# Kernel optimization log

Hardware: AMD Instinct MI355X
Metric: run time of the kernel (lower is better)

Reference implementation:

```python
import jax, jax.numpy as jnp
import numpy as np

N_NODES = 100000
N_EDGES = 1600000
IN_FEATS = 128
HIDDEN = 32
HEADS = 4
OUT_FEATS = 64
NEG_SLOPE = 0.2  # DGL GATConv default negative_slope


def gat_layer(x, src, dst, fc_w, attn_l, attn_r, bias, n_nodes):
    """DGL GATConv: fc -> per-node attn terms -> edge leaky_relu -> segment softmax -> scatter-sum.
    x: [N, F_in]; fc_w: [F_in, H*D]; attn_l/attn_r: [H, D]; bias: [H*D].
    Returns [N, H, D]."""
    H, D = attn_l.shape
    feat = (x @ fc_w).reshape(-1, H, D)            # [N, H, D]
    el = jnp.sum(feat * attn_l, axis=-1)           # [N, H]
    er = jnp.sum(feat * attn_r, axis=-1)           # [N, H]
    e = jax.nn.leaky_relu(el[src] + er[dst], NEG_SLOPE)   # [E, H]
    # segment softmax over incoming edges of each dst node
    m = jax.ops.segment_max(e, dst, num_segments=n_nodes)  # [N, H] (-inf for 0-in-degree)
    ex = jnp.exp(e - m[dst])                       # [E, H]
    denom = jax.ops.segment_sum(ex, dst, num_segments=n_nodes)  # [N, H]
    alpha = ex / denom[dst]                        # [E, H]
    msg = feat[src] * alpha[:, :, None]            # [E, H, D]
    out = jax.ops.segment_sum(msg, dst, num_segments=n_nodes)   # [N, H, D]
    return out + bias.reshape(1, H, D)


def setup_inputs() -> dict:
    key = jax.random.key(0)
    ks = jax.random.split(key, 12)
    features = jax.random.normal(ks[0], (N_NODES, IN_FEATS), dtype=jnp.float32)
    src = jax.random.randint(ks[1], (N_EDGES,), 0, N_NODES)
    dst = jax.random.randint(ks[2], (N_EDGES,), 0, N_NODES)
    s1 = 1.0 / np.sqrt(IN_FEATS)
    s2 = 1.0 / np.sqrt(HIDDEN * HEADS)
    fc1_w = jax.random.normal(ks[3], (IN_FEATS, HIDDEN * HEADS), dtype=jnp.float32) * s1
    attn_l1 = jax.random.normal(ks[4], (HEADS, HIDDEN), dtype=jnp.float32) * s1
    attn_r1 = jax.random.normal(ks[5], (HEADS, HIDDEN), dtype=jnp.float32) * s1
    bias1 = jnp.zeros((HIDDEN * HEADS,), dtype=jnp.float32)
    fc2_w = jax.random.normal(ks[6], (HIDDEN * HEADS, OUT_FEATS), dtype=jnp.float32) * s2
    attn_l2 = jax.random.normal(ks[7], (1, OUT_FEATS), dtype=jnp.float32) * s2
    attn_r2 = jax.random.normal(ks[8], (1, OUT_FEATS), dtype=jnp.float32) * s2
    bias2 = jnp.zeros((OUT_FEATS,), dtype=jnp.float32)
    return {"features": features, "src": src, "dst": dst,
            "fc1_w": fc1_w, "attn_l1": attn_l1, "attn_r1": attn_r1, "bias1": bias1,
            "fc2_w": fc2_w, "attn_l2": attn_l2, "attn_r2": attn_r2, "bias2": bias2}


def reference(features, src, dst, fc1_w, attn_l1, attn_r1, bias1, fc2_w, attn_l2, attn_r2, bias2):
    n = features.shape[0]
    x = gat_layer(features, src, dst, fc1_w, attn_l1, attn_r1, bias1, n)  # [N, H, D1]
    x = jax.nn.elu(x.reshape(n, -1))                                     # [N, H*D1]
    x = gat_layer(x, src, dst, fc2_w, attn_l2, attn_r2, bias2, n)        # [N, 1, D2]
    return x.mean(axis=1)                                                # [N, D2]
```

## Files before the change

kernel.cpp:

```cpp
#include <hip/hip_runtime.h>
#include <math.h>

typedef __attribute__((ext_vector_type(8))) short bf16x8;
typedef __attribute__((ext_vector_type(4))) float f32x4;

#define MAXDEG 64


__device__ __forceinline__ unsigned int packbf2(float a, float b) {
    unsigned int ua = __float_as_uint(a);
    ua = (ua + 0x7FFFu + ((ua >> 16) & 1u)) >> 16;
    unsigned int ub = __float_as_uint(b);
    ub = (ub + 0x7FFFu + ((ub >> 16) & 1u)) & 0xFFFF0000u;
    return ua | ub;
}

__device__ __forceinline__ unsigned short bf16r(float x) {
    unsigned int u = __float_as_uint(x);
    u = (u + 0x7FFFu + ((u >> 16) & 1u)) >> 16;
    return (unsigned short)u;
}

__device__ __forceinline__ void bf2_fma(unsigned int u, float w, float& a0, float& a1) {
    a0 += w * __uint_as_float(u << 16);
    a1 += w * __uint_as_float(u & 0xFFFF0000u);
}


__global__ __launch_bounds__(256) void k_gemm1_rank(const int* __restrict__ dst,
                                                    int* __restrict__ cnt,
                                                    int* __restrict__ rank, int e,
                                                    const float* __restrict__ X,
                                                    const float* __restrict__ W,
                                                    const float* __restrict__ attn_l,
                                                    const float* __restrict__ attn_r,
                                                    unsigned short* __restrict__ feat,
                                                    float* __restrict__ el,
                                                    float* __restrict__ er, int n) {
    __shared__ unsigned short sX[64 * 128];
    __shared__ unsigned short sWT[128 * 128];
    int t = threadIdx.x;
    int ebase = blockIdx.x * 1024 + t;
    int d0 = (ebase < e) ? dst[ebase] : -1;
    int d1 = (ebase + 256 < e) ? dst[ebase + 256] : -1;
    int d2 = (ebase + 512 < e) ? dst[ebase + 512] : -1;
    int d3 = (ebase + 768 < e) ? dst[ebase + 768] : -1;

    int node0 = blockIdx.x * 64;
    {
        const float4* Xv = (const float4*)X;
        char* sXb = (char*)sX;
        for (int i = t; i < 2048; i += 256) {
            int r = i >> 5, q = i & 31;
            int node = node0 + r;
            float4 val = make_float4(0.f, 0.f, 0.f, 0.f);
            if (node < n) val = Xv[(size_t)node * 32 + q];
            unsigned off = (unsigned)(r * 256 + q * 8) ^ (unsigned)((r & 7) << 4);
            *(uint2*)(sXb + off) = make_uint2(packbf2(val.x, val.y), packbf2(val.z, val.w));
        }
    }
    {
        char* sWb = (char*)sWT;
        int c = t & 127;
        int kp0 = (t >> 7) * 32;
        for (int j = 0; j < 32; ++j) {
            int kp = kp0 + j;
            float f0 = W[(2 * kp) * 128 + c];
            float f1 = W[(2 * kp + 1) * 128 + c];
            unsigned off = (unsigned)(c * 256 + kp * 4) ^ (unsigned)((c & 7) << 4);
            *(unsigned*)(sWb + off) = packbf2(f0, f1);
        }
    }
    __syncthreads();
    int p0 = 0, p1 = 0, p2 = 0, p3 = 0;
    if (d0 >= 0) p0 = atomicAdd(&cnt[d0], 1);
    if (d1 >= 0) p1 = atomicAdd(&cnt[d1], 1);
    if (d2 >= 0) p2 = atomicAdd(&cnt[d2], 1);
    if (d3 >= 0) p3 = atomicAdd(&cnt[d3], 1);

    int w = t >> 6;
    int l = t & 63;
    int lr = l & 15;
    int lk = l >> 4;
    f32x4 acc[8] = {};
    {
        const char* sXb = (const char*)sX;
        const char* sWb = (const char*)sWT;
        int arow = w * 16 + lr;
        unsigned aswz = (unsigned)((arow & 7) << 4);
        unsigned abase = (unsigned)(arow * 256 + lk * 16);
#pragma unroll
        for (int kb = 0; kb < 4; ++kb) {
            bf16x8 afrag = *(const bf16x8*)(sXb + ((abase + kb * 64) ^ aswz));
#pragma unroll
            for (int cb = 0; cb < 8; ++cb) {
                int col = cb * 16 + lr;
                unsigned boff = (unsigned)(col * 256 + kb * 64 + lk * 16) ^ (unsigned)((col & 7) << 4);
                bf16x8 bfrag = *(const bf16x8*)(sWb + boff);
                acc[cb] = __builtin_amdgcn_mfma_f32_16x16x32_bf16(afrag, bfrag, acc[cb], 0, 0, 0);
            }
        }
    }
    {
        float alv[8], arv[8];
#pragma unroll
        for (int cb = 0; cb < 8; ++cb) {
            alv[cb] = attn_l[cb * 16 + lr];
            arv[cb] = attn_r[cb * 16 + lr];
        }
#pragma unroll
        for (int r = 0; r < 4; ++r) {
            int node = node0 + w * 16 + lk * 4 + r;
            float pl[4], pr[4];
#pragma unroll
            for (int h = 0; h < 4; ++h) {
                pl[h] = acc[2 * h][r] * alv[2 * h] + acc[2 * h + 1][r] * alv[2 * h + 1];
                pr[h] = acc[2 * h][r] * arv[2 * h] + acc[2 * h + 1][r] * arv[2 * h + 1];
            }
#pragma unroll
            for (int off = 1; off < 16; off <<= 1) {
#pragma unroll
                for (int h = 0; h < 4; ++h) {
                    pl[h] += __shfl_xor(pl[h], off);
                    pr[h] += __shfl_xor(pr[h], off);
                }
            }
            if (node < n && lr < 4) {
                el[node * 4 + lr] = pl[lr];
                er[node * 4 + lr] = pr[lr];
            }
        }
    }
    if (d0 >= 0) rank[ebase] = p0;
    if (d1 >= 0) rank[ebase + 256] = p1;
    if (d2 >= 0) rank[ebase + 512] = p2;
    if (d3 >= 0) rank[ebase + 768] = p3;

    __syncthreads();
    unsigned short* sOut = sWT;
#pragma unroll
    for (int cb = 0; cb < 8; ++cb)
#pragma unroll
        for (int r = 0; r < 4; ++r)
            sOut[(w * 16 + lk * 4 + r) * 128 + cb * 16 + lr] = bf16r(acc[cb][r]);
    __syncthreads();
    for (int i = t; i < 1024; i += 256) {
        int r = i >> 4, q = i & 15;
        int node = node0 + r;
        if (node < n)
            *(uint4*)(feat + (size_t)node * 128 + q * 8) = *(const uint4*)(sOut + r * 128 + q * 8);
    }
}


__global__ __launch_bounds__(256) void k_place(const int* __restrict__ src,
                                               const int* __restrict__ dst,
                                               const int* __restrict__ rank,
                                               int* __restrict__ csrF, int e) {
    int base = blockIdx.x * 1024 + threadIdx.x;
#pragma unroll
    for (int j = 0; j < 4; ++j) {
        int i = base + j * 256;
        if (i < e) {
            int r = rank[i];
            if (r < MAXDEG) csrF[(size_t)dst[i] * MAXDEG + r] = src[i];
        }
    }
}


__global__ __launch_bounds__(256) void k_gemm2(const float* __restrict__ X,
                                               const float* __restrict__ W,
                                               const float* __restrict__ attn_l,
                                               const float* __restrict__ attn_r,
                                               unsigned short* __restrict__ feat,
                                               float* __restrict__ el,
                                               float* __restrict__ er, int n) {
    __shared__ unsigned short sX[64 * 128];
    __shared__ unsigned short sWT[64 * 128];
    int t = threadIdx.x;
    int node0 = blockIdx.x * 64;
    {
        const float4* Xv = (const float4*)X;
        char* sXb = (char*)sX;
        for (int i = t; i < 2048; i += 256) {
            int r = i >> 5, q = i & 31;
            int node = node0 + r;
            float4 val = make_float4(0.f, 0.f, 0.f, 0.f);
            if (node < n) val = Xv[(size_t)node * 32 + q];
            unsigned off = (unsigned)(r * 256 + q * 8) ^ (unsigned)((r & 7) << 4);
            *(uint2*)(sXb + off) = make_uint2(packbf2(val.x, val.y), packbf2(val.z, val.w));
        }
    }
    {
        char* sWb = (char*)sWT;
        int c = t & 63;
        int kp0 = (t >> 6) * 16;
#pragma unroll
        for (int j = 0; j < 16; ++j) {
            int kp = kp0 + j;
            float f0 = W[(2 * kp) * 64 + c];
            float f1 = W[(2 * kp + 1) * 64 + c];
            unsigned off = (unsigned)(c * 256 + kp * 4) ^ (unsigned)((c & 7) << 4);
            *(unsigned*)(sWb + off) = packbf2(f0, f1);
        }
    }
    __syncthreads();

    int w = t >> 6;
    int l = t & 63;
    int lr = l & 15;
    int lk = l >> 4;
    f32x4 acc[4] = {};
    {
        const char* sXb = (const char*)sX;
        const char* sWb = (const char*)sWT;
        int arow = w * 16 + lr;
        unsigned aswz = (unsigned)((arow & 7) << 4);
        unsigned abase = (unsigned)(arow * 256 + lk * 16);
#pragma unroll
        for (int kb = 0; kb < 4; ++kb) {
            bf16x8 afrag = *(const bf16x8*)(sXb + ((abase + kb * 64) ^ aswz));
#pragma unroll
            for (int cb = 0; cb < 4; ++cb) {
                int col = cb * 16 + lr;
                unsigned boff = (unsigned)(col * 256 + kb * 64 + lk * 16) ^ (unsigned)((col & 7) << 4);
                bf16x8 bfrag = *(const bf16x8*)(sWb + boff);
                acc[cb] = __builtin_amdgcn_mfma_f32_16x16x32_bf16(afrag, bfrag, acc[cb], 0, 0, 0);
            }
        }
    }
    {
        float alv[4], arv[4];
#pragma unroll
        for (int cb = 0; cb < 4; ++cb) {
            alv[cb] = attn_l[cb * 16 + lr];
            arv[cb] = attn_r[cb * 16 + lr];
        }
#pragma unroll
        for (int r = 0; r < 4; ++r) {
            int node = node0 + w * 16 + lk * 4 + r;
            float pl = 0.f, pr = 0.f;
#pragma unroll
            for (int cb = 0; cb < 4; ++cb) {
                pl += acc[cb][r] * alv[cb];
                pr += acc[cb][r] * arv[cb];
            }
#pragma unroll
            for (int off = 1; off < 16; off <<= 1) {
                pl += __shfl_xor(pl, off);
                pr += __shfl_xor(pr, off);
            }
            if (node < n && lr == 0) {
                el[node] = pl;
                er[node] = pr;
            }
        }
    }
    __syncthreads();
    unsigned short* sOut = sWT;
#pragma unroll
    for (int cb = 0; cb < 4; ++cb)
#pragma unroll
        for (int r = 0; r < 4; ++r)
            sOut[(w * 16 + lk * 4 + r) * 64 + cb * 16 + lr] = bf16r(acc[cb][r]);
    __syncthreads();
    for (int i = t; i < 512; i += 256) {
        int r = i >> 3, q = i & 7;
        int node = node0 + r;
        if (node < n)
            *(uint4*)(feat + (size_t)node * 64 + q * 8) = *(const uint4*)(sOut + r * 64 + q * 8);
    }
}


__global__ __launch_bounds__(256) void k_gather1(const int* __restrict__ cnt,
                                                 const int* __restrict__ csrF,
                                                 const unsigned short* __restrict__ feat,
                                                 const float* __restrict__ el,
                                                 const float* __restrict__ er,
                                                 const float* __restrict__ bias,
                                                 float* __restrict__ xout, int n) {
    int wid = (blockIdx.x * blockDim.x + threadIdx.x) >> 6;
    int lane = threadIdx.x & 63;
    if (wid >= n) return;
    int g = lane >> 4;
    int dl = lane & 15;
    int h = dl >> 2;
    int deg = cnt[wid];
    if (deg > MAXDEG) deg = MAXDEG;
    int start = wid * MAXDEG, end = start + deg;
    float erh = er[wid * 4 + h];
    float A[8] = {};
    float D = 0.f;
    int slot = start + g;
    for (; slot + 12 < end; slot += 16) {
        int s0 = csrF[slot];
        int s1 = csrF[slot + 4];
        int s2 = csrF[slot + 8];
        int s3 = csrF[slot + 12];
        float e0 = el[s0 * 4 + h];
        float e1 = el[s1 * 4 + h];
        float e2 = el[s2 * 4 + h];
        float e3 = el[s3 * 4 + h];
        uint4 f0 = *(const uint4*)(feat + (size_t)s0 * 128 + 8 * dl);
        uint4 f1 = *(const uint4*)(feat + (size_t)s1 * 128 + 8 * dl);
        uint4 f2 = *(const uint4*)(feat + (size_t)s2 * 128 + 8 * dl);
        uint4 f3 = *(const uint4*)(feat + (size_t)s3 * 128 + 8 * dl);
        e0 += erh; e0 = (e0 > 0.f) ? e0 : 0.2f * e0; float w0 = __expf(e0);
        e1 += erh; e1 = (e1 > 0.f) ? e1 : 0.2f * e1; float w1 = __expf(e1);
        e2 += erh; e2 = (e2 > 0.f) ? e2 : 0.2f * e2; float w2 = __expf(e2);
        e3 += erh; e3 = (e3 > 0.f) ? e3 : 0.2f * e3; float w3 = __expf(e3);
        D += w0 + w1 + w2 + w3;
        bf2_fma(f0.x, w0, A[0], A[1]); bf2_fma(f0.y, w0, A[2], A[3]);
        bf2_fma(f0.z, w0, A[4], A[5]); bf2_fma(f0.w, w0, A[6], A[7]);
        bf2_fma(f1.x, w1, A[0], A[1]); bf2_fma(f1.y, w1, A[2], A[3]);
        bf2_fma(f1.z, w1, A[4], A[5]); bf2_fma(f1.w, w1, A[6], A[7]);
        bf2_fma(f2.x, w2, A[0], A[1]); bf2_fma(f2.y, w2, A[2], A[3]);
        bf2_fma(f2.z, w2, A[4], A[5]); bf2_fma(f2.w, w2, A[6], A[7]);
        bf2_fma(f3.x, w3, A[0], A[1]); bf2_fma(f3.y, w3, A[2], A[3]);
        bf2_fma(f3.z, w3, A[4], A[5]); bf2_fma(f3.w, w3, A[6], A[7]);
    }
    for (; slot < end; slot += 4) {
        int s = csrF[slot];
        float e0 = el[s * 4 + h];
        uint4 f = *(const uint4*)(feat + (size_t)s * 128 + 8 * dl);
        e0 += erh; e0 = (e0 > 0.f) ? e0 : 0.2f * e0; float w = __expf(e0);
        D += w;
        bf2_fma(f.x, w, A[0], A[1]); bf2_fma(f.y, w, A[2], A[3]);
        bf2_fma(f.z, w, A[4], A[5]); bf2_fma(f.w, w, A[6], A[7]);
    }
#pragma unroll
    for (int off = 16; off < 64; off <<= 1) {
#pragma unroll
        for (int j = 0; j < 8; ++j) A[j] += __shfl_xor(A[j], off);
        D += __shfl_xor(D, off);
    }
    if (g == 0) {
        float rd = (D > 0.f) ? 1.f / D : 0.f;
        const float* bp = bias + 8 * dl;
        float4 b0 = *(const float4*)bp;
        float4 b1 = *(const float4*)(bp + 4);
        float o[8];
        o[0] = A[0] * rd + b0.x; o[1] = A[1] * rd + b0.y;
        o[2] = A[2] * rd + b0.z; o[3] = A[3] * rd + b0.w;
        o[4] = A[4] * rd + b1.x; o[5] = A[5] * rd + b1.y;
        o[6] = A[6] * rd + b1.z; o[7] = A[7] * rd + b1.w;
#pragma unroll
        for (int j = 0; j < 8; ++j) o[j] = (o[j] > 0.f) ? o[j] : (__expf(o[j]) - 1.f);
        float* xp = xout + (size_t)wid * 128 + 8 * dl;
        *(float4*)xp = make_float4(o[0], o[1], o[2], o[3]);
        *(float4*)(xp + 4) = make_float4(o[4], o[5], o[6], o[7]);
    }
}


__global__ __launch_bounds__(256) void k_gather2(const int* __restrict__ cnt,
                                                 const int* __restrict__ csrF,
                                                 const unsigned short* __restrict__ feat,
                                                 const float* __restrict__ el,
                                                 const float* __restrict__ er,
                                                 const float* __restrict__ bias,
                                                 float* __restrict__ out, int n) {
    int wid = (blockIdx.x * blockDim.x + threadIdx.x) >> 6;
    int lane = threadIdx.x & 63;
    if (wid >= n) return;
    int g = lane >> 3;
    int dl = lane & 7;
    int deg = cnt[wid];
    if (deg > MAXDEG) deg = MAXDEG;
    int start = wid * MAXDEG, end = start + deg;
    float erv = er[wid];
    float A[8] = {};
    float D = 0.f;
    int slot = start + g;
    for (; slot + 8 < end; slot += 16) {
        int s0 = csrF[slot];
        int s1 = csrF[slot + 8];
        float e0 = el[s0];
        float e1 = el[s1];
        uint4 f0 = *(const uint4*)(feat + (size_t)s0 * 64 + 8 * dl);
        uint4 f1 = *(const uint4*)(feat + (size_t)s1 * 64 + 8 * dl);
        e0 += erv; e0 = (e0 > 0.f) ? e0 : 0.2f * e0; float w0 = __expf(e0);
        e1 += erv; e1 = (e1 > 0.f) ? e1 : 0.2f * e1; float w1 = __expf(e1);
        D += w0 + w1;
        bf2_fma(f0.x, w0, A[0], A[1]); bf2_fma(f0.y, w0, A[2], A[3]);
        bf2_fma(f0.z, w0, A[4], A[5]); bf2_fma(f0.w, w0, A[6], A[7]);
        bf2_fma(f1.x, w1, A[0], A[1]); bf2_fma(f1.y, w1, A[2], A[3]);
        bf2_fma(f1.z, w1, A[4], A[5]); bf2_fma(f1.w, w1, A[6], A[7]);
    }
    if (slot < end) {
        int s = csrF[slot];
        float e0 = el[s];
        uint4 f = *(const uint4*)(feat + (size_t)s * 64 + 8 * dl);
        e0 += erv; e0 = (e0 > 0.f) ? e0 : 0.2f * e0; float w = __expf(e0);
        D += w;
        bf2_fma(f.x, w, A[0], A[1]); bf2_fma(f.y, w, A[2], A[3]);
        bf2_fma(f.z, w, A[4], A[5]); bf2_fma(f.w, w, A[6], A[7]);
    }
#pragma unroll
    for (int off = 8; off < 64; off <<= 1) {
#pragma unroll
        for (int j = 0; j < 8; ++j) A[j] += __shfl_xor(A[j], off);
        D += __shfl_xor(D, off);
    }
    if (g == 0) {
        float rd = (D > 0.f) ? 1.f / D : 0.f;
        const float* bp = bias + 8 * dl;
        float4 b0 = *(const float4*)bp;
        float4 b1 = *(const float4*)(bp + 4);
        float4 o0, o1;
        o0.x = A[0] * rd + b0.x; o0.y = A[1] * rd + b0.y;
        o0.z = A[2] * rd + b0.z; o0.w = A[3] * rd + b0.w;
        o1.x = A[4] * rd + b1.x; o1.y = A[5] * rd + b1.y;
        o1.z = A[6] * rd + b1.z; o1.w = A[7] * rd + b1.w;
        float* op = out + (size_t)wid * 64 + 8 * dl;
        *(float4*)op = o0;
        *(float4*)(op + 4) = o1;
    }
}


extern "C" void kernel_launch(void* const* d_in, const int* in_sizes, int n_in,
                              void* d_out, int out_size, void* d_ws, size_t ws_size,
                              hipStream_t stream) {
    const float* features = (const float*)d_in[0];
    const int* src = (const int*)d_in[1];
    const int* dst = (const int*)d_in[2];
    const float* fc1_w = (const float*)d_in[3];
    const float* attn_l1 = (const float*)d_in[4];
    const float* attn_r1 = (const float*)d_in[5];
    const float* bias1 = (const float*)d_in[6];
    const float* fc2_w = (const float*)d_in[7];
    const float* attn_l2 = (const float*)d_in[8];
    const float* attn_r2 = (const float*)d_in[9];
    const float* bias2 = (const float*)d_in[10];
    const int N = in_sizes[0] / 128;
    const int E = in_sizes[1];

    char* ws = (char*)d_ws;
    size_t off = 0;
    auto alloc = [&](size_t bytes) {
        void* p = ws + off;
        off = (off + bytes + 255) & ~(size_t)255;
        return p;
    };
    int* cnt = (int*)alloc((size_t)N * 4);
    int* rank = (int*)alloc((size_t)E * 4);
    int* csrF = (int*)alloc((size_t)N * MAXDEG * 4);
    float* x2 = (float*)alloc((size_t)N * 128 * 4);
    size_t l1_off = off;
    unsigned short* feat1 = (unsigned short*)alloc((size_t)N * 128 * 2);
    float* el1 = (float*)alloc((size_t)N * 4 * 4);
    float* er1 = (float*)alloc((size_t)N * 4 * 4);
    off = l1_off;
    unsigned short* feat2 = (unsigned short*)alloc((size_t)N * 64 * 2);
    float* el2 = (float*)alloc((size_t)N * 4);
    float* er2 = (float*)alloc((size_t)N * 4);

    hipMemsetAsync(cnt, 0, (size_t)N * 4, stream);

    int ngemm = (N + 63) / 64;
    int nrank = (E + 1023) / 1024;
    int nblk = (ngemm > nrank) ? ngemm : nrank;
    k_gemm1_rank<<<nblk, 256, 0, stream>>>(dst, cnt, rank, E,
                                           features, fc1_w, attn_l1, attn_r1,
                                           feat1, el1, er1, N);
    k_place<<<(E + 1023) / 1024, 256, 0, stream>>>(src, dst, rank, csrF, E);

    int nwave = (N + 3) / 4;
    k_gather1<<<nwave, 256, 0, stream>>>(cnt, csrF, feat1, el1, er1, bias1, x2, N);
    k_gemm2<<<(N + 63) / 64, 256, 0, stream>>>(x2, fc2_w, attn_l2, attn_r2, feat2, el2, er2, N);
    k_gather2<<<nwave, 256, 0, stream>>>(cnt, csrF, feat2, el2, er2, bias2, (float*)d_out, N);
}
```

Before: 249.3 us.

## Fuse CSR placement into gemm1 kernel and pad degree counters

Removes the separate k_place kernel and the rank array: the fused gemm1 kernel now loads src alongside dst and writes each edge's source directly into the padded CSR slot right after its atomic increment. Degree counters are spaced CPAD ints apart so each node's counter sits on its own cache line, reducing atomic contention between neighbouring nodes. The trade-off is a 16x larger counter array to memset and read with strided access in the gather kernels, plus extra register pressure in the gemm kernel.

```diff
diff --git a/kernel.cpp b/kernel.cpp
--- a/kernel.cpp
+++ b/kernel.cpp
@@ -5,6 +5,7 @@
 typedef __attribute__((ext_vector_type(4))) float f32x4;
 
 #define MAXDEG 64
+#define CPAD 16
 
 
 __device__ __forceinline__ unsigned int packbf2(float a, float b) {
@@ -27,16 +28,17 @@
 }
 
 
-__global__ __launch_bounds__(256) void k_gemm1_rank(const int* __restrict__ dst,
-                                                    int* __restrict__ cnt,
-                                                    int* __restrict__ rank, int e,
-                                                    const float* __restrict__ X,
-                                                    const float* __restrict__ W,
-                                                    const float* __restrict__ attn_l,
-                                                    const float* __restrict__ attn_r,
-                                                    unsigned short* __restrict__ feat,
-                                                    float* __restrict__ el,
-                                                    float* __restrict__ er, int n) {
+__global__ __launch_bounds__(256) void k_gemm1_csr(const int* __restrict__ src,
+                                                   const int* __restrict__ dst,
+                                                   int* __restrict__ cnt,
+                                                   int* __restrict__ csrF, int e,
+                                                   const float* __restrict__ X,
+                                                   const float* __restrict__ W,
+                                                   const float* __restrict__ attn_l,
+                                                   const float* __restrict__ attn_r,
+                                                   unsigned short* __restrict__ feat,
+                                                   float* __restrict__ el,
+                                                   float* __restrict__ er, int n) {
     __shared__ unsigned short sX[64 * 128];
     __shared__ unsigned short sWT[128 * 128];
     int t = threadIdx.x;
@@ -45,6 +47,10 @@
     int d1 = (ebase + 256 < e) ? dst[ebase + 256] : -1;
     int d2 = (ebase + 512 < e) ? dst[ebase + 512] : -1;
     int d3 = (ebase + 768 < e) ? dst[ebase + 768] : -1;
+    int sv0 = (ebase < e) ? src[ebase] : 0;
+    int sv1 = (ebase + 256 < e) ? src[ebase + 256] : 0;
+    int sv2 = (ebase + 512 < e) ? src[ebase + 512] : 0;
+    int sv3 = (ebase + 768 < e) ? src[ebase + 768] : 0;
 
     int node0 = blockIdx.x * 64;
     {
@@ -73,10 +79,10 @@
     }
     __syncthreads();
     int p0 = 0, p1 = 0, p2 = 0, p3 = 0;
-    if (d0 >= 0) p0 = atomicAdd(&cnt[d0], 1);
-    if (d1 >= 0) p1 = atomicAdd(&cnt[d1], 1);
-    if (d2 >= 0) p2 = atomicAdd(&cnt[d2], 1);
-    if (d3 >= 0) p3 = atomicAdd(&cnt[d3], 1);
+    if (d0 >= 0) p0 = atomicAdd(&cnt[d0 * CPAD], 1);
+    if (d1 >= 0) p1 = atomicAdd(&cnt[d1 * CPAD], 1);
+    if (d2 >= 0) p2 = atomicAdd(&cnt[d2 * CPAD], 1);
+    if (d3 >= 0) p3 = atomicAdd(&cnt[d3 * CPAD], 1);
 
     int w = t >> 6;
     int l = t & 63;
@@ -101,6 +107,11 @@
             }
         }
     }
+    if (d0 >= 0 && p0 < MAXDEG) csrF[(size_t)d0 * MAXDEG + p0] = sv0;
+    if (d1 >= 0 && p1 < MAXDEG) csrF[(size_t)d1 * MAXDEG + p1] = sv1;
+    if (d2 >= 0 && p2 < MAXDEG) csrF[(size_t)d2 * MAXDEG + p2] = sv2;
+    if (d3 >= 0 && p3 < MAXDEG) csrF[(size_t)d3 * MAXDEG + p3] = sv3;
+
     {
         float alv[8], arv[8];
 #pragma unroll
@@ -131,10 +142,6 @@
             }
         }
     }
-    if (d0 >= 0) rank[ebase] = p0;
-    if (d1 >= 0) rank[ebase + 256] = p1;
-    if (d2 >= 0) rank[ebase + 512] = p2;
-    if (d3 >= 0) rank[ebase + 768] = p3;
 
     __syncthreads();
     unsigned short* sOut = sWT;
@@ -149,22 +156,6 @@
         int node = node0 + r;
         if (node < n)
             *(uint4*)(feat + (size_t)node * 128 + q * 8) = *(const uint4*)(sOut + r * 128 + q * 8);
-    }
-}
-
-
-__global__ __launch_bounds__(256) void k_place(const int* __restrict__ src,
-                                               const int* __restrict__ dst,
-                                               const int* __restrict__ rank,
-                                               int* __restrict__ csrF, int e) {
-    int base = blockIdx.x * 1024 + threadIdx.x;
-#pragma unroll
-    for (int j = 0; j < 4; ++j) {
-        int i = base + j * 256;
-        if (i < e) {
-            int r = rank[i];
-            if (r < MAXDEG) csrF[(size_t)dst[i] * MAXDEG + r] = src[i];
-        }
     }
 }
 
@@ -287,7 +278,7 @@
     int g = lane >> 4;
     int dl = lane & 15;
     int h = dl >> 2;
-    int deg = cnt[wid];
+    int deg = cnt[wid * CPAD];
     if (deg > MAXDEG) deg = MAXDEG;
     int start = wid * MAXDEG, end = start + deg;
     float erh = er[wid * 4 + h];
@@ -367,7 +358,7 @@
     if (wid >= n) return;
     int g = lane >> 3;
     int dl = lane & 7;
-    int deg = cnt[wid];
+    int deg = cnt[wid * CPAD];
     if (deg > MAXDEG) deg = MAXDEG;
     int start = wid * MAXDEG, end = start + deg;
     float erv = er[wid];
@@ -445,8 +436,7 @@
         off = (off + bytes + 255) & ~(size_t)255;
         return p;
     };
-    int* cnt = (int*)alloc((size_t)N * 4);
-    int* rank = (int*)alloc((size_t)E * 4);
+    int* cnt = (int*)alloc((size_t)N * CPAD * 4);
     int* csrF = (int*)alloc((size_t)N * MAXDEG * 4);
     float* x2 = (float*)alloc((size_t)N * 128 * 4);
     size_t l1_off = off;
@@ -458,15 +448,14 @@
     float* el2 = (float*)alloc((size_t)N * 4);
     float* er2 = (float*)alloc((size_t)N * 4);
 
-    hipMemsetAsync(cnt, 0, (size_t)N * 4, stream);
+    hipMemsetAsync(cnt, 0, (size_t)N * CPAD * 4, stream);
 
     int ngemm = (N + 63) / 64;
-    int nrank = (E + 1023) / 1024;
-    int nblk = (ngemm > nrank) ? ngemm : nrank;
-    k_gemm1_rank<<<nblk, 256, 0, stream>>>(dst, cnt, rank, E,
-                                           features, fc1_w, attn_l1, attn_r1,
-                                           feat1, el1, er1, N);
-    k_place<<<(E + 1023) / 1024, 256, 0, stream>>>(src, dst, rank, csrF, E);
+    int nedge = (E + 1023) / 1024;
+    int nblk = (ngemm > nedge) ? ngemm : nedge;
+    k_gemm1_csr<<<nblk, 256, 0, stream>>>(src, dst, cnt, csrF, E,
+                                          features, fc1_w, attn_l1, attn_r1,
+                                          feat1, el1, er1, N);
 
     int nwave = (N + 3) / 4;
     k_gather1<<<nwave, 256, 0, stream>>>(cnt, csrF, feat1, el1, er1, bias1, x2, N);
```

Measured after the change: 269.5 us. 8.1% more time.

## Partition degree-count atomics into 8 copies and store layer-1 output as bf16

Applied to the files above, without the earlier changes.

Degree counting now spreads its atomics over 8 partitioned counter arrays, chosen by block index, so fewer updates collide on the same address. A new merge kernel computes per-partition base offsets and the total count, and the placement step adds that base to the rank. Separately, the ELU output of layer 1 is written as packed bf16 instead of fp32, which halves that buffer's write and read traffic and removes the conversion in gemm2. The cost is an extra kernel launch, an 8x larger counter memset, and the merge pass's own memory traffic.

```diff
diff --git a/kernel.cpp b/kernel.cpp
--- a/kernel.cpp
+++ b/kernel.cpp
@@ -5,6 +5,7 @@
 typedef __attribute__((ext_vector_type(4))) float f32x4;
 
 #define MAXDEG 64
+#define NPART 8
 
 
 __device__ __forceinline__ unsigned int packbf2(float a, float b) {
@@ -28,7 +29,7 @@
 
 
 __global__ __launch_bounds__(256) void k_gemm1_rank(const int* __restrict__ dst,
-                                                    int* __restrict__ cnt,
+                                                    int* __restrict__ cnt8,
                                                     int* __restrict__ rank, int e,
                                                     const float* __restrict__ X,
                                                     const float* __restrict__ W,
@@ -41,6 +42,7 @@
     __shared__ unsigned short sWT[128 * 128];
     int t = threadIdx.x;
     int ebase = blockIdx.x * 1024 + t;
+    int* cpart = cnt8 + (size_t)(blockIdx.x & (NPART - 1)) * n;
     int d0 = (ebase < e) ? dst[ebase] : -1;
     int d1 = (ebase + 256 < e) ? dst[ebase + 256] : -1;
     int d2 = (ebase + 512 < e) ? dst[ebase + 512] : -1;
@@ -73,10 +75,10 @@
     }
     __syncthreads();
     int p0 = 0, p1 = 0, p2 = 0, p3 = 0;
-    if (d0 >= 0) p0 = atomicAdd(&cnt[d0], 1);
-    if (d1 >= 0) p1 = atomicAdd(&cnt[d1], 1);
-    if (d2 >= 0) p2 = atomicAdd(&cnt[d2], 1);
-    if (d3 >= 0) p3 = atomicAdd(&cnt[d3], 1);
+    if (d0 >= 0) p0 = atomicAdd(&cpart[d0], 1);
+    if (d1 >= 0) p1 = atomicAdd(&cpart[d1], 1);
+    if (d2 >= 0) p2 = atomicAdd(&cpart[d2], 1);
+    if (d3 >= 0) p3 = atomicAdd(&cpart[d3], 1);
 
     int w = t >> 6;
     int l = t & 63;
@@ -153,23 +155,44 @@
 }
 
 
+__global__ __launch_bounds__(256) void k_merge(const int* __restrict__ cnt8,
+                                               int* __restrict__ base8,
+                                               int* __restrict__ cnt, int n) {
+    int i = blockIdx.x * 256 + threadIdx.x;
+    if (i >= n) return;
+    int s = 0;
+    int b[NPART];
+#pragma unroll
+    for (int p = 0; p < NPART; ++p) {
+        b[p] = s;
+        s += cnt8[(size_t)p * n + i];
+    }
+    cnt[i] = s;
+#pragma unroll
+    for (int p = 0; p < NPART; ++p) base8[i * NPART + p] = b[p];
+}
+
+
 __global__ __launch_bounds__(256) void k_place(const int* __restrict__ src,
                                                const int* __restrict__ dst,
                                                const int* __restrict__ rank,
+                                               const int* __restrict__ base8,
                                                int* __restrict__ csrF, int e) {
     int base = blockIdx.x * 1024 + threadIdx.x;
 #pragma unroll
     for (int j = 0; j < 4; ++j) {
         int i = base + j * 256;
         if (i < e) {
-            int r = rank[i];
-            if (r < MAXDEG) csrF[(size_t)dst[i] * MAXDEG + r] = src[i];
-        }
-    }
-}
-
-
-__global__ __launch_bounds__(256) void k_gemm2(const float* __restrict__ X,
+            int part = (i >> 10) & (NPART - 1);
+            int d = dst[i];
+            int slot = base8[d * NPART + part] + rank[i];
+            if (slot < MAXDEG) csrF[(size_t)d * MAXDEG + slot] = src[i];
+        }
+    }
+}
+
+
+__global__ __launch_bounds__(256) void k_gemm2(const unsigned short* __restrict__ X2,
                                                const float* __restrict__ W,
                                                const float* __restrict__ attn_l,
                                                const float* __restrict__ attn_r,
@@ -181,15 +204,15 @@
     int t = threadIdx.x;
     int node0 = blockIdx.x * 64;
     {
-        const float4* Xv = (const float4*)X;
+        const uint2* Xv = (const uint2*)X2;
         char* sXb = (char*)sX;
         for (int i = t; i < 2048; i += 256) {
             int r = i >> 5, q = i & 31;
             int node = node0 + r;
-            float4 val = make_float4(0.f, 0.f, 0.f, 0.f);
+            uint2 val = make_uint2(0u, 0u);
             if (node < n) val = Xv[(size_t)node * 32 + q];
             unsigned off = (unsigned)(r * 256 + q * 8) ^ (unsigned)((r & 7) << 4);
-            *(uint2*)(sXb + off) = make_uint2(packbf2(val.x, val.y), packbf2(val.z, val.w));
+            *(uint2*)(sXb + off) = val;
         }
     }
     {
@@ -280,7 +303,7 @@
                                                  const float* __restrict__ el,
                                                  const float* __restrict__ er,
                                                  const float* __restrict__ bias,
-                                                 float* __restrict__ xout, int n) {
+                                                 unsigned short* __restrict__ xout, int n) {
     int wid = (blockIdx.x * blockDim.x + threadIdx.x) >> 6;
     int lane = threadIdx.x & 63;
     if (wid >= n) return;
@@ -348,9 +371,12 @@
         o[6] = A[6] * rd + b1.z; o[7] = A[7] * rd + b1.w;
 #pragma unroll
         for (int j = 0; j < 8; ++j) o[j] = (o[j] > 0.f) ? o[j] : (__expf(o[j]) - 1.f);
-        float* xp = xout + (size_t)wid * 128 + 8 * dl;
-        *(float4*)xp = make_float4(o[0], o[1], o[2], o[3]);
-        *(float4*)(xp + 4) = make_float4(o[4], o[5], o[6], o[7]);
+        uint4 pk;
+        pk.x = packbf2(o[0], o[1]);
+        pk.y = packbf2(o[2], o[3]);
+        pk.z = packbf2(o[4], o[5]);
+        pk.w = packbf2(o[6], o[7]);
+        *(uint4*)(xout + (size_t)wid * 128 + 8 * dl) = pk;
     }
 }
 
@@ -445,10 +471,12 @@
         off = (off + bytes + 255) & ~(size_t)255;
         return p;
     };
+    int* cnt8 = (int*)alloc((size_t)N * NPART * 4);
+    int* base8 = (int*)alloc((size_t)N * NPART * 4);
     int* cnt = (int*)alloc((size_t)N * 4);
     int* rank = (int*)alloc((size_t)E * 4);
     int* csrF = (int*)alloc((size_t)N * MAXDEG * 4);
-    float* x2 = (float*)alloc((size_t)N * 128 * 4);
+    unsigned short* x2 = (unsigned short*)alloc((size_t)N * 128 * 2);
     size_t l1_off = off;
     unsigned short* feat1 = (unsigned short*)alloc((size_t)N * 128 * 2);
     float* el1 = (float*)alloc((size_t)N * 4 * 4);
@@ -458,15 +486,16 @@
     float* el2 = (float*)alloc((size_t)N * 4);
     float* er2 = (float*)alloc((size_t)N * 4);
 
-    hipMemsetAsync(cnt, 0, (size_t)N * 4, stream);
+    hipMemsetAsync(cnt8, 0, (size_t)N * NPART * 4, stream);
 
     int ngemm = (N + 63) / 64;
-    int nrank = (E + 1023) / 1024;
-    int nblk = (ngemm > nrank) ? ngemm : nrank;
-    k_gemm1_rank<<<nblk, 256, 0, stream>>>(dst, cnt, rank, E,
+    int nedge = (E + 1023) / 1024;
+    int nblk = (ngemm > nedge) ? ngemm : nedge;
+    k_gemm1_rank<<<nblk, 256, 0, stream>>>(dst, cnt8, rank, E,
                                            features, fc1_w, attn_l1, attn_r1,
                                            feat1, el1, er1, N);
-    k_place<<<(E + 1023) / 1024, 256, 0, stream>>>(src, dst, rank, csrF, E);
+    k_merge<<<(N + 255) / 256, 256, 0, stream>>>(cnt8, base8, cnt, N);
+    k_place<<<(E + 1023) / 1024, 256, 0, stream>>>(src, dst, rank, base8, csrF, E);
 
     int nwave = (N + 3) / 4;
     k_gather1<<<nwave, 256, 0, stream>>>(cnt, csrF, feat1, el1, er1, bias1, x2, N);
```

After: 258.2 us. 1.04x slower.
